# Kernel optimization log

Measured on AMD Instinct MI355X. Metric: run time of the kernel, lower is better.

The kernel has to match this reference:

```python
import jax, jax.numpy as jnp
import numpy as np

MARGIN = 0.3
N, D = 8192, 1024
NUM_IDS = 751

def setup_inputs() -> dict:
    key = jax.random.key(0)
    k1, k2 = jax.random.split(key)
    inputs = jax.random.normal(k1, (N, D), dtype=jnp.float32)
    targets = jax.random.randint(k2, (N,), 0, NUM_IDS, dtype=jnp.int64)
    return {"inputs": inputs, "targets": targets}

def reference(inputs, targets):
    # sim[i,j] = <x_i, x_j>
    sim = jnp.matmul(inputs, inputs.T)  # [N, N]
    same = targets[:, None] == targets[None, :]  # [N, N] bool
    # positives: same label AND sim < 1 -> contribute (1 - sim)
    pos_mask = same & (sim < 1.0)
    pos_loss = jnp.sum(jnp.where(pos_mask, 1.0 - sim, 0.0), axis=1)  # [N]
    # negatives: different label AND sim > margin -> contribute sim
    neg_mask = (~same) & (sim > MARGIN)
    neg_loss = jnp.sum(jnp.where(neg_mask, sim, 0.0), axis=1)  # [N]
    n = inputs.shape[0]
    return jnp.sum(pos_loss + neg_loss) / n
```

## Files before the change

### kernel.cpp

```cpp
#include <hip/hip_runtime.h>
#include <stdint.h>

typedef float f32x4 __attribute__((ext_vector_type(4)));

#define NROWS 8192
#define DIM   1024
#define BK    128
#define NKT   (DIM / BK)
#define MARGIN 0.3f

#define GLOAD_LDS16(gp, lp)                                                    \
  __builtin_amdgcn_global_load_lds(                                            \
      (const __attribute__((address_space(1))) void*)(gp),                     \
      (__attribute__((address_space(3))) void*)(lp), 16, 0, 0)

__global__ __launch_bounds__(256) void cvt_f32_fp8(const float* __restrict__ in,
                                                   uint8_t* __restrict__ out,
                                                   float* __restrict__ loss) {
  if (blockIdx.x == 0 && threadIdx.x == 0) loss[0] = 0.0f;
  size_t i = ((size_t)blockIdx.x * 256 + threadIdx.x) * 16;
  float4 v0 = *(const float4*)(in + i);
  float4 v1 = *(const float4*)(in + i + 4);
  float4 v2 = *(const float4*)(in + i + 8);
  float4 v3 = *(const float4*)(in + i + 12);
  int w0 = 0, w1 = 0, w2 = 0, w3 = 0;
  w0 = __builtin_amdgcn_cvt_pk_fp8_f32(v0.x, v0.y, w0, false);
  w0 = __builtin_amdgcn_cvt_pk_fp8_f32(v0.z, v0.w, w0, true);
  w1 = __builtin_amdgcn_cvt_pk_fp8_f32(v1.x, v1.y, w1, false);
  w1 = __builtin_amdgcn_cvt_pk_fp8_f32(v1.z, v1.w, w1, true);
  w2 = __builtin_amdgcn_cvt_pk_fp8_f32(v2.x, v2.y, w2, false);
  w2 = __builtin_amdgcn_cvt_pk_fp8_f32(v2.z, v2.w, w2, true);
  w3 = __builtin_amdgcn_cvt_pk_fp8_f32(v3.x, v3.y, w3, false);
  w3 = __builtin_amdgcn_cvt_pk_fp8_f32(v3.z, v3.w, w3, true);
  uint4 p; p.x = (unsigned)w0; p.y = (unsigned)w1; p.z = (unsigned)w2; p.w = (unsigned)w3;
  *(uint4*)(out + i) = p;
}

__global__ __launch_bounds__(256, 3) void gram_loss(const uint8_t* __restrict__ A8,
                                                    const int* __restrict__ targets,
                                                    float* __restrict__ out) {
  __shared__ uint8_t As[128 * 128];
  __shared__ uint8_t Bs[128 * 128];
  __shared__ int tRow[128];
  __shared__ int tCol[128];
  __shared__ float wsum[4];

  const int pos = (blockIdx.x & 7) * 260 + (blockIdx.x >> 3);
  int q = 0, pre = 0;
  if (pos >= 136)  { q = 1; pre = 136; }
  if (pos >= 392)  { q = 2; pre = 392; }
  if (pos >= 648)  { q = 3; pre = 648; }
  if (pos >= 904)  { q = 4; pre = 904; }
  if (pos >= 1040) { q = 5; pre = 1040; }
  if (pos >= 1296) { q = 6; pre = 1296; }
  if (pos >= 1552) { q = 7; pre = 1552; }
  if (pos >= 1688) { q = 8; pre = 1688; }
  if (pos >= 1944) { q = 9; pre = 1944; }
  const int r  = pos - pre;
  const int Si = (q >= 4) + (q >= 7) + (q >= 9);
  const int Sj = Si + (q - (Si * 4 - (Si * (Si - 1)) / 2));
  int li, lj;
  if (Si == Sj) {
    li = (r>=16)+(r>=31)+(r>=45)+(r>=58)+(r>=70)+(r>=81)+(r>=91)+(r>=100)
       + (r>=108)+(r>=115)+(r>=121)+(r>=126)+(r>=130)+(r>=133)+(r>=135);
    lj = li + (r - (li * (33 - li)) / 2);
  } else {
    li = r >> 4;
    lj = r & 15;
  }
  const int bi = Si * 16 + li;
  const int bj = Sj * 16 + lj;

  const int iBase = bi * 128;
  const int jBase = bj * 128;

  const int tid  = threadIdx.x;
  const int wave = tid >> 6;
  const int lane = tid & 63;

  if (tid < 128) tRow[tid] = targets[iBase + tid];
  else           tCol[tid - 128] = targets[jBase + tid - 128];

  const int lrow = lane >> 3;
  const int cg   = (lane & 7) ^ lrow;
  const uint8_t* gA = A8 + (size_t)(iBase + wave * 32 + lrow) * DIM + cg * 16;
  const uint8_t* gB = A8 + (size_t)(jBase + wave * 32 + lrow) * DIM + cg * 16;
  uint8_t* lA = &As[wave * 32 * 128];
  uint8_t* lB = &Bs[wave * 32 * 128];

  const int m0 = (wave >> 1) * 64;
  const int n0 = (wave & 1) * 64;
  const int fr = lane & 15;
  const int h  = lane >> 4;
  const int r7 = fr & 7;
  const int hHi = h >> 1;
  const int hLo = (h & 1) * 8;

  f32x4 acc[4][4] = {};

#define STAGE(kt_)                                                             \
  { const int kO_ = (kt_) * BK;                                                \
    _Pragma("unroll")                                                          \
    for (int l = 0; l < 4; ++l)                                                \
      GLOAD_LDS16(gA + (size_t)(l * 8) * DIM + kO_, lA + l * 8 * 128);         \
    _Pragma("unroll")                                                          \
    for (int l = 0; l < 4; ++l)                                                \
      GLOAD_LDS16(gB + (size_t)(l * 8) * DIM + kO_, lB + l * 8 * 128); }

  STAGE(0);
  asm volatile("s_waitcnt vmcnt(0)" ::: "memory");
  __builtin_amdgcn_s_barrier();

  for (int kt = 0; kt < NKT; ++kt) {
    long af[4][4], bf[4][4];
#pragma unroll
    for (int ks = 0; ks < 4; ++ks) {
      const int colOff = (((ks * 2 + hHi) ^ r7) * 16) + hLo;
#pragma unroll
      for (int mi = 0; mi < 4; ++mi)
        af[ks][mi] = *(const long*)&As[(m0 + mi * 16 + fr) * 128 + colOff];
#pragma unroll
      for (int ni = 0; ni < 4; ++ni)
        bf[ks][ni] = *(const long*)&Bs[(n0 + ni * 16 + fr) * 128 + colOff];
    }
    asm volatile("s_waitcnt lgkmcnt(0)" ::: "memory");
    __builtin_amdgcn_s_barrier();
    if (kt + 1 < NKT) STAGE(kt + 1);
    __builtin_amdgcn_sched_barrier(0);
#pragma unroll
    for (int ks = 0; ks < 4; ++ks)
#pragma unroll
      for (int mi = 0; mi < 4; ++mi)
#pragma unroll
        for (int ni = 0; ni < 4; ++ni)
          acc[mi][ni] = __builtin_amdgcn_mfma_f32_16x16x32_fp8_fp8(
              af[ks][mi], bf[ks][ni], acc[mi][ni], 0, 0, 0);
    __builtin_amdgcn_sched_barrier(0);
    asm volatile("s_waitcnt vmcnt(0)" ::: "memory");
    __builtin_amdgcn_s_barrier();
  }
#undef STAGE

  const int col = lane & 15;
  const int rquad = (lane >> 4) * 4;
  float lsum = 0.0f;
#pragma unroll
  for (int ni = 0; ni < 4; ++ni) {
    const int tj = tCol[n0 + ni * 16 + col];
#pragma unroll
    for (int mi = 0; mi < 4; ++mi) {
#pragma unroll
      for (int r2 = 0; r2 < 4; ++r2) {
        float s = acc[mi][ni][r2];
        int ti = tRow[m0 + mi * 16 + rquad + r2];
        lsum += (ti == tj) ? (s < 1.0f ? 1.0f - s : 0.0f)
                           : (s > MARGIN ? s : 0.0f);
      }
    }
  }
  if (bi != bj) lsum *= 2.0f;

#pragma unroll
  for (int off = 32; off > 0; off >>= 1) lsum += __shfl_down(lsum, off, 64);
  if (lane == 0) wsum[wave] = lsum;
  __syncthreads();
  if (tid == 0)
    atomicAdd(out, (wsum[0] + wsum[1] + wsum[2] + wsum[3]) * (1.0f / (float)NROWS));
}

extern "C" void kernel_launch(void* const* d_in, const int* in_sizes, int n_in,
                              void* d_out, int out_size, void* d_ws, size_t ws_size,
                              hipStream_t stream) {
  const float* x = (const float*)d_in[0];
  const int* targets = (const int*)d_in[1];
  float* out = (float*)d_out;
  uint8_t* x8 = (uint8_t*)d_ws;

  cvt_f32_fp8<<<2048, 256, 0, stream>>>(x, x8, out);
  gram_loss<<<2080, 256, 0, stream>>>(x8, targets, out);
}
```

Measured before the change: 136.7 us.

## Drop register-prefetch pipeline, use 16-byte LDS fragment reads, raise occupancy

The software pipeline is removed: it held a full K-tile of fragments in registers while the next global-to-LDS stage was issued. Each K-tile is now loaded between two block barriers and then consumed in two halves using 16-byte LDS reads, each feeding two FP8 MFMAs. The launch-bounds minimum blocks per CU goes from 3 to 4. The aim is to cut register pressure so more blocks fit and latency is hidden across blocks instead of within one. The cost is that a block no longer overlaps its own global loads with its MFMA work.

```diff
diff --git a/kernel.cpp b/kernel.cpp
--- a/kernel.cpp
+++ b/kernel.cpp
@@ -2,6 +2,7 @@
 #include <stdint.h>
 
 typedef float f32x4 __attribute__((ext_vector_type(4)));
+typedef long  v2l   __attribute__((ext_vector_type(2)));
 
 #define NROWS 8192
 #define DIM   1024
@@ -36,7 +37,7 @@
   *(uint4*)(out + i) = p;
 }
 
-__global__ __launch_bounds__(256, 3) void gram_loss(const uint8_t* __restrict__ A8,
+__global__ __launch_bounds__(256, 4) void gram_loss(const uint8_t* __restrict__ A8,
                                                     const int* __restrict__ targets,
                                                     float* __restrict__ out) {
   __shared__ uint8_t As[128 * 128];
@@ -93,53 +94,43 @@
   const int fr = lane & 15;
   const int h  = lane >> 4;
   const int r7 = fr & 7;
-  const int hHi = h >> 1;
-  const int hLo = (h & 1) * 8;
+  const int s0 = ((h    ) ^ r7) * 16;
+  const int s1 = ((h + 4) ^ r7) * 16;
 
   f32x4 acc[4][4] = {};
 
-#define STAGE(kt_)                                                             \
-  { const int kO_ = (kt_) * BK;                                                \
-    _Pragma("unroll")                                                          \
-    for (int l = 0; l < 4; ++l)                                                \
-      GLOAD_LDS16(gA + (size_t)(l * 8) * DIM + kO_, lA + l * 8 * 128);         \
-    _Pragma("unroll")                                                          \
-    for (int l = 0; l < 4; ++l)                                                \
-      GLOAD_LDS16(gB + (size_t)(l * 8) * DIM + kO_, lB + l * 8 * 128); }
+  for (int kt = 0; kt < NKT; ++kt) {
+    __syncthreads();
+    const int kOff = kt * BK;
+#pragma unroll
+    for (int l = 0; l < 4; ++l)
+      GLOAD_LDS16(gA + (size_t)(l * 8) * DIM + kOff, lA + l * 8 * 128);
+#pragma unroll
+    for (int l = 0; l < 4; ++l)
+      GLOAD_LDS16(gB + (size_t)(l * 8) * DIM + kOff, lB + l * 8 * 128);
+    __syncthreads();
 
-  STAGE(0);
-  asm volatile("s_waitcnt vmcnt(0)" ::: "memory");
-  __builtin_amdgcn_s_barrier();
-
-  for (int kt = 0; kt < NKT; ++kt) {
-    long af[4][4], bf[4][4];
 #pragma unroll
-    for (int ks = 0; ks < 4; ++ks) {
-      const int colOff = (((ks * 2 + hHi) ^ r7) * 16) + hLo;
+    for (int rr = 0; rr < 2; ++rr) {
+      const int so = rr ? s1 : s0;
+      v2l a[4], b[4];
 #pragma unroll
       for (int mi = 0; mi < 4; ++mi)
-        af[ks][mi] = *(const long*)&As[(m0 + mi * 16 + fr) * 128 + colOff];
+        a[mi] = *(const v2l*)&As[(m0 + mi * 16 + fr) * 128 + so];
 #pragma unroll
       for (int ni = 0; ni < 4; ++ni)
-        bf[ks][ni] = *(const long*)&Bs[(n0 + ni * 16 + fr) * 128 + colOff];
-    }
-    asm volatile("s_waitcnt lgkmcnt(0)" ::: "memory");
-    __builtin_amdgcn_s_barrier();
-    if (kt + 1 < NKT) STAGE(kt + 1);
-    __builtin_amdgcn_sched_barrier(0);
-#pragma unroll
-    for (int ks = 0; ks < 4; ++ks)
+        b[ni] = *(const v2l*)&Bs[(n0 + ni * 16 + fr) * 128 + so];
 #pragma unroll
       for (int mi = 0; mi < 4; ++mi)
 #pragma unroll
-        for (int ni = 0; ni < 4; ++ni)
+        for (int ni = 0; ni < 4; ++ni) {
           acc[mi][ni] = __builtin_amdgcn_mfma_f32_16x16x32_fp8_fp8(
-              af[ks][mi], bf[ks][ni], acc[mi][ni], 0, 0, 0);
-    __builtin_amdgcn_sched_barrier(0);
-    asm volatile("s_waitcnt vmcnt(0)" ::: "memory");
-    __builtin_amdgcn_s_barrier();
+              a[mi].x, b[ni].x, acc[mi][ni], 0, 0, 0);
+          acc[mi][ni] = __builtin_amdgcn_mfma_f32_16x16x32_fp8_fp8(
+              a[mi].y, b[ni].y, acc[mi][ni], 0, 0, 0);
+        }
+    }
   }
-#undef STAGE
 
   const int col = lane & 15;
   const int rquad = (lane >> 4) * 4;
```

Result: faster. 126.2 us (-7.7%).
